# Kernel tuning notes

Hardware: AMD Instinct MI355X
Metric: run time of the kernel (lower is better)

The kernel has to match this reference:

```python
import jax, jax.numpy as jnp
import numpy as np

B, S, H, F, E, K = 2, 2048, 1024, 4096, 8, 2
NH = H // 128  # heads of dim 128, per SimpleMoEBlock.__init__
DH = H // NH


def _layernorm(x, g, b, eps=1e-5):
    m = x.mean(-1, keepdims=True)
    v = ((x - m) ** 2).mean(-1, keepdims=True)
    return (x - m) / jnp.sqrt(v + eps) * g + b


def _forward(x, ln_attn_g, ln_attn_b, ln_mlp_g, ln_mlp_b,
             in_proj_w, in_proj_b, out_proj_w, out_proj_b,
             router_w, fc1_w, fc1_b, fc2_w, fc2_b):
    # --- self attention (nn.MultiheadAttention, batch_first, no mask) ---
    xa = _layernorm(x, ln_attn_g, ln_attn_b)                    # [B,S,H]
    qkv = xa @ in_proj_w.T + in_proj_b                          # [B,S,3H]
    q, k, v = jnp.split(qkv, 3, axis=-1)
    def heads(t):
        return t.reshape(B, S, NH, DH).transpose(0, 2, 1, 3)    # [B,NH,S,DH]
    q, k, v = heads(q), heads(k), heads(v)
    scores = jnp.einsum('bhqd,bhkd->bhqk', q, k) / jnp.sqrt(jnp.asarray(DH, x.dtype))
    attn = jnp.einsum('bhqk,bhkd->bhqd', jax.nn.softmax(scores, axis=-1), v)
    attn = attn.transpose(0, 2, 1, 3).reshape(B, S, H)
    attn = attn @ out_proj_w.T + out_proj_b
    h = x + attn                                                # residual

    # --- MoE feed-forward ---
    y = _layernorm(h, ln_mlp_g, ln_mlp_b).reshape(B * S, H)     # flat tokens [T,H]
    logits = y @ router_w.T                                     # [T,E]
    probs = jax.nn.softmax(logits, axis=-1)
    top_scores, top_idx = jax.lax.top_k(probs, K)               # [T,K]
    # per-token per-expert combine weight; 0 for unrouted tokens -> identical
    # math to torch's index_select/index_add dispatch
    w = (jax.nn.one_hot(top_idx, E, dtype=y.dtype) * top_scores[..., None]).sum(axis=1)  # [T,E]

    combined = jnp.zeros_like(y)
    for e in range(E):  # fixed small expert count
        he = jax.nn.silu(y @ fc1_w[e].T + fc1_b[e])             # [T,F]
        oe = he @ fc2_w[e].T + fc2_b[e]                         # [T,H]
        combined = combined + oe * w[:, e:e + 1]
    return h + combined.reshape(B, S, H)


def setup_inputs() -> dict:
    key = jax.random.key(0)
    ks = jax.random.split(key, 8)
    s = 0.02
    return {
        'x': jax.random.normal(ks[0], (B, S, H), jnp.float32),
        'ln_attn_g': jnp.ones((H,), jnp.float32),
        'ln_attn_b': jnp.zeros((H,), jnp.float32),
        'ln_mlp_g': jnp.ones((H,), jnp.float32),
        'ln_mlp_b': jnp.zeros((H,), jnp.float32),
        'in_proj_w': jax.random.normal(ks[1], (3 * H, H), jnp.float32) * s,
        'in_proj_b': jnp.zeros((3 * H,), jnp.float32),
        'out_proj_w': jax.random.normal(ks[2], (H, H), jnp.float32) * s,
        'out_proj_b': jnp.zeros((H,), jnp.float32),
        'router_w': jax.random.normal(ks[3], (E, H), jnp.float32) * s,
        'fc1_w': jax.random.normal(ks[4], (E, F, H), jnp.float32) * s,
        'fc1_b': jnp.zeros((E, F), jnp.float32),
        'fc2_w': jax.random.normal(ks[5], (E, H, F), jnp.float32) * s,
        'fc2_b': jnp.zeros((E, H), jnp.float32),
    }


def reference(x, ln_attn_g, ln_attn_b, ln_mlp_g, ln_mlp_b,
              in_proj_w, in_proj_b, out_proj_w, out_proj_b,
              router_w, fc1_w, fc1_b, fc2_w, fc2_b):
    return _forward(x, ln_attn_g, ln_attn_b, ln_mlp_g, ln_mlp_b,
                    in_proj_w, in_proj_b, out_proj_w, out_proj_b,
                    router_w, fc1_w, fc1_b, fc2_w, fc2_b)
```

## Files before the change

kernel.cpp:

```cpp
#include <hip/hip_runtime.h>

#define T_TOK 4096
#define S_SEQ 2048
#define H_DIM 1024
#define H3    3072
#define NHEAD 8
#define DHEAD 128
#define F_DIM 4096
#define NEXP  8
#define MAX_RB 72
#define NSLOT 9216

typedef __bf16 bf16x8 __attribute__((ext_vector_type(8)));
typedef float  f32x4  __attribute__((ext_vector_type(4)));
typedef __attribute__((address_space(1))) const unsigned int* gas1_t;
typedef __attribute__((address_space(3))) unsigned int* las3_t;

__device__ __forceinline__ unsigned short f2bf(float f){
  unsigned int u = __builtin_bit_cast(unsigned int, f);
  u += 0x7fffu + ((u>>16)&1u);
  return (unsigned short)(u>>16);
}
__device__ __forceinline__ float bf2f(unsigned short h){
  unsigned int u = ((unsigned int)h)<<16;
  return __builtin_bit_cast(float, u);
}
__device__ __forceinline__ f32x4 MF(bf16x8 a, bf16x8 b, f32x4 c){
  return __builtin_amdgcn_mfma_f32_16x16x32_bf16(a,b,c,0,0,0);
}
__device__ __forceinline__ void gload16(const void* g, void* l){
  __builtin_amdgcn_global_load_lds((gas1_t)g, (las3_t)l, 16, 0, 0);
}
__device__ __forceinline__ float blockReduceSum(float v){
  __shared__ float sh_red[4];
  #pragma unroll
  for(int o=32;o>0;o>>=1) v += __shfl_down(v,o,64);
  int w = threadIdx.x>>6;
  if((threadIdx.x&63)==0) sh_red[w]=v;
  __syncthreads();
  float tot = sh_red[0]+sh_red[1]+sh_red[2]+sh_red[3];
  __syncthreads();
  return tot;
}

__global__ __launch_bounds__(256) void k_ln_split(const float* __restrict__ x,
    const float* __restrict__ g, const float* __restrict__ bta,
    unsigned short* __restrict__ hi, unsigned short* __restrict__ lo){
  int t = blockIdx.x, tid = threadIdx.x;
  float4 v = reinterpret_cast<const float4*>(x + (size_t)t*H_DIM)[tid];
  float mean = blockReduceSum(v.x+v.y+v.z+v.w) * (1.0f/H_DIM);
  float d0=v.x-mean,d1=v.y-mean,d2=v.z-mean,d3=v.w-mean;
  float var = blockReduceSum(d0*d0+d1*d1+d2*d2+d3*d3) * (1.0f/H_DIM);
  float rstd = rsqrtf(var + 1e-5f);
  float4 gv = reinterpret_cast<const float4*>(g)[tid];
  float4 bv = reinterpret_cast<const float4*>(bta)[tid];
  float o0=d0*rstd*gv.x+bv.x, o1=d1*rstd*gv.y+bv.y, o2=d2*rstd*gv.z+bv.z, o3=d3*rstd*gv.w+bv.w;
  size_t base = (size_t)t*H_DIM + tid*4;
  unsigned short h0=f2bf(o0),h1=f2bf(o1),h2=f2bf(o2),h3=f2bf(o3);
  *reinterpret_cast<ushort4*>(hi+base) = make_ushort4(h0,h1,h2,h3);
  *reinterpret_cast<ushort4*>(lo+base) = make_ushort4(
      f2bf(o0-bf2f(h0)), f2bf(o1-bf2f(h1)), f2bf(o2-bf2f(h2)), f2bf(o3-bf2f(h3)));
}

__global__ __launch_bounds__(256) void k_wsplit(const float* __restrict__ w,
    unsigned short* __restrict__ hi, unsigned short* __restrict__ lo, int n4){
  int i = blockIdx.x*256 + threadIdx.x;
  if(i>=n4) return;
  float4 v = reinterpret_cast<const float4*>(w)[i];
  size_t base = (size_t)i*4;
  unsigned short h0=f2bf(v.x),h1=f2bf(v.y),h2=f2bf(v.z),h3=f2bf(v.w);
  *reinterpret_cast<ushort4*>(hi+base) = make_ushort4(h0,h1,h2,h3);
  *reinterpret_cast<ushort4*>(lo+base) = make_ushort4(
      f2bf(v.x-bf2f(h0)), f2bf(v.y-bf2f(h1)), f2bf(v.z-bf2f(h2)), f2bf(v.w-bf2f(h3)));
}

__global__ __launch_bounds__(256) void k_wconv(const float* __restrict__ w,
    unsigned short* __restrict__ hi, int n4){
  int i = blockIdx.x*256 + threadIdx.x;
  if(i>=n4) return;
  float4 v = reinterpret_cast<const float4*>(w)[i];
  *reinterpret_cast<ushort4*>(hi + (size_t)i*4) =
      make_ushort4(f2bf(v.x), f2bf(v.y), f2bf(v.z), f2bf(v.w));
}

template<int EPI>
__global__ __launch_bounds__(256) void k_gemm_split(
    const unsigned short* __restrict__ Ah, const unsigned short* __restrict__ Al,
    const unsigned short* __restrict__ Bh, const unsigned short* __restrict__ Bl,
    const float* __restrict__ bias, const float* __restrict__ resid,
    unsigned short* __restrict__ Chi, unsigned short* __restrict__ Clo,
    float* __restrict__ Cf, int N, int Kd){
  int m0 = blockIdx.y*128, n0 = blockIdx.x*128;
  int tid=threadIdx.x, wid=tid>>6, lane=tid&63, lr=lane&15, lg=lane>>4;
  int wr=wid>>1, wc=wid&1;
  __shared__ unsigned short tAh[4096], tAl[4096], tBh[4096], tBl[4096];
  f32x4 acc[4][4] = {};
  for(int k0=0;k0<Kd;k0+=32){
    #pragma unroll
    for(int i=0;i<2;i++){
      int p = i*256 + tid;
      int row = p>>2, pc = p&3;
      int lc = pc ^ ((row>>1)&3);
      size_t go = (size_t)row*Kd + k0 + lc*8;
      int lb = (i*256 + wid*64)*8;
      gload16(Ah + (size_t)m0*Kd + go, tAh + lb);
      gload16(Al + (size_t)m0*Kd + go, tAl + lb);
      gload16(Bh + (size_t)n0*Kd + go, tBh + lb);
      gload16(Bl + (size_t)n0*Kd + go, tBl + lb);
    }
    asm volatile("s_waitcnt vmcnt(0)" ::: "memory");
    __syncthreads();
    bf16x8 ah[4], al[4], bh[4], bl[4];
    #pragma unroll
    for(int q=0;q<4;q++){
      int ra = wr*64+q*16+lr;
      int ia = ra*32 + ((lg ^ ((ra>>1)&3))<<3);
      ah[q] = *reinterpret_cast<const bf16x8*>(&tAh[ia]);
      al[q] = *reinterpret_cast<const bf16x8*>(&tAl[ia]);
      int rb = wc*64+q*16+lr;
      int ib = rb*32 + ((lg ^ ((rb>>1)&3))<<3);
      bh[q] = *reinterpret_cast<const bf16x8*>(&tBh[ib]);
      bl[q] = *reinterpret_cast<const bf16x8*>(&tBl[ib]);
    }
    #pragma unroll
    for(int mf=0;mf<4;mf++)
      #pragma unroll
      for(int nf=0;nf<4;nf++){
        acc[mf][nf] = MF(ah[mf], bh[nf], acc[mf][nf]);
        acc[mf][nf] = MF(ah[mf], bl[nf], acc[mf][nf]);
        acc[mf][nf] = MF(al[mf], bh[nf], acc[mf][nf]);
      }
    __syncthreads();
  }
  #pragma unroll
  for(int mf=0;mf<4;mf++)
    #pragma unroll
    for(int nf=0;nf<4;nf++)
      #pragma unroll
      for(int r=0;r<4;r++){
        int row = m0 + wr*64 + mf*16 + lg*4 + r;
        int col = n0 + wc*64 + nf*16 + lr;
        float v = acc[mf][nf][r] + bias[col];
        size_t idx = (size_t)row*N + col;
        if(EPI==0){
          unsigned short hb = f2bf(v);
          Chi[idx]=hb; Clo[idx]=f2bf(v-bf2f(hb));
        } else {
          Cf[idx] = v + resid[idx];
        }
      }
}

__global__ __launch_bounds__(256) void k_vtrans(const unsigned short* __restrict__ qh,
    const unsigned short* __restrict__ ql,
    unsigned short* __restrict__ vth, unsigned short* __restrict__ vtl){
  int bh = blockIdx.z, d0 = blockIdx.y*32, s0 = blockIdx.x*32;
  int b = bh>>3, hh = bh&7;
  int tid=threadIdx.x;
  __shared__ unsigned short th[32][40], tl[32][40];
  int sr = tid>>3, dc = (tid&7)*4;
  size_t src = ((size_t)(b*S_SEQ + s0 + sr))*H3 + 2*H_DIM + hh*DHEAD + d0 + dc;
  *reinterpret_cast<ushort4*>(&th[sr][dc]) = *reinterpret_cast<const ushort4*>(qh+src);
  *reinterpret_cast<ushort4*>(&tl[sr][dc]) = *reinterpret_cast<const ushort4*>(ql+src);
  __syncthreads();
  int dr = tid>>3, sc = (tid&7)*4;
  size_t dst = ((size_t)(bh*DHEAD) + d0+dr)*S_SEQ + s0 + sc;
  *reinterpret_cast<ushort4*>(vth+dst) = make_ushort4(th[sc][dr],th[sc+1][dr],th[sc+2][dr],th[sc+3][dr]);
  *reinterpret_cast<ushort4*>(vtl+dst) = make_ushort4(tl[sc][dr],tl[sc+1][dr],tl[sc+2][dr],tl[sc+3][dr]);
}

__global__ __launch_bounds__(256,1) void k_attn(const unsigned short* __restrict__ qkv_hi,
    const unsigned short* __restrict__ qkv_lo,
    const unsigned short* __restrict__ vt_hi, const unsigned short* __restrict__ vt_lo,
    float* __restrict__ opb, float* __restrict__ mlb, int kv_span){
  const float SCALE = 0.08838834764831843f;
  int qb = blockIdx.x, bh = blockIdx.y, zz = blockIdx.z;
  int b = bh>>3, hh = bh&7;
  int kvbase = zz*kv_span, kvend = kvbase + kv_span;
  int tid=threadIdx.x, wid=tid>>6, lane=tid&63, lr=lane&15, lg=lane>>4;
  __shared__ unsigned short kh[2][4096], kl[2][4096], vh[2][4096], vl[2][4096];
  __shared__ unsigned short ph[4][1024], pl[4][1024];
  int row0 = qb*128 + wid*32;
  bf16x8 qh_[2][4], ql_[2][4];
  #pragma unroll
  for(int j=0;j<2;j++){
    size_t qbase = ((size_t)(b*S_SEQ) + row0 + j*16 + lr)*H3 + hh*DHEAD;
    #pragma unroll
    for(int kk=0;kk<4;kk++){
      qh_[j][kk] = *reinterpret_cast<const bf16x8*>(qkv_hi + qbase + kk*32 + lg*8);
      ql_[j][kk] = *reinterpret_cast<const bf16x8*>(qkv_lo + qbase + kk*32 + lg*8);
    }
  }
  f32x4 o_acc[2][8] = {};
  float mrun[2] = {-1e30f,-1e30f};
  float lrun[2] = {0.f,0.f};

  auto STAGE = [&](int buf, int kv0){
    #pragma unroll
    for(int i=0;i<2;i++){
      int p = i*256 + tid;
      int lb = (i*256 + wid*64)*8;
      {
        int krow = p>>4, pc = p&15;
        int lc = (pc&8)|((pc&7)^(krow&7));
        size_t go = ((size_t)(b*S_SEQ + kv0 + krow))*H3 + H_DIM + hh*DHEAD + lc*8;
        gload16(qkv_hi + go, &kh[buf][lb]);
        gload16(qkv_lo + go, &kl[buf][lb]);
      }
      {
        int vrow = p>>2, pc = p&3;
        int lc = pc ^ ((vrow>>1)&3);
        size_t gv = ((size_t)(bh*DHEAD) + vrow)*S_SEQ + kv0 + lc*8;
        gload16(vt_hi + gv, &vh[buf][lb]);
        gload16(vt_lo + gv, &vl[buf][lb]);
      }
    }
  };

  STAGE(0, kvbase);
  asm volatile("s_waitcnt vmcnt(0)" ::: "memory");
  __syncthreads();
  int cur = 0;
  for(int kv0=kvbase; kv0<kvend; kv0+=32){
    if(kv0+32 < kvend) STAGE(cur^1, kv0+32);
    f32x4 s0[2] = {}, s1[2] = {};
    #pragma unroll
    for(int kk=0;kk<4;kk++){
      int c = kk*4+lg;
      int phys = (c&8)|((c&7)^(lr&7));
      bf16x8 kah = *reinterpret_cast<const bf16x8*>(&kh[cur][lr*128 + phys*8]);
      bf16x8 kal = *reinterpret_cast<const bf16x8*>(&kl[cur][lr*128 + phys*8]);
      bf16x8 kbh = *reinterpret_cast<const bf16x8*>(&kh[cur][(16+lr)*128 + phys*8]);
      bf16x8 kbl = *reinterpret_cast<const bf16x8*>(&kl[cur][(16+lr)*128 + phys*8]);
      #pragma unroll
      for(int j=0;j<2;j++){
        s0[j] = MF(kah, qh_[j][kk], s0[j]);
        s0[j] = MF(kah, ql_[j][kk], s0[j]);
        s0[j] = MF(kal, qh_[j][kk], s0[j]);
        s1[j] = MF(kbh, qh_[j][kk], s1[j]);
        s1[j] = MF(kbh, ql_[j][kk], s1[j]);
        s1[j] = MF(kbl, qh_[j][kk], s1[j]);
      }
    }
    float sc[2][8]; float mt[2];
    #pragma unroll
    for(int j=0;j<2;j++){
      #pragma unroll
      for(int r=0;r<4;r++){ sc[j][r] = s0[j][r]*SCALE; sc[j][4+r] = s1[j][r]*SCALE; }
      float m_ = fmaxf(fmaxf(fmaxf(sc[j][0],sc[j][1]),fmaxf(sc[j][2],sc[j][3])),
                       fmaxf(fmaxf(sc[j][4],sc[j][5]),fmaxf(sc[j][6],sc[j][7])));
      m_ = fmaxf(m_, __shfl_xor(m_,16,64));
      m_ = fmaxf(m_, __shfl_xor(m_,32,64));
      mt[j] = m_;
    }
    int skip = __all((mt[0] <= mrun[0]+8.0f) && (mt[1] <= mrun[1]+8.0f));
    if(!skip){
      #pragma unroll
      for(int j=0;j<2;j++){
        float mn = fmaxf(mrun[j], mt[j]);
        float rs = __expf(mrun[j]-mn);
        lrun[j] *= rs; mrun[j] = mn;
        #pragma unroll
        for(int nf2=0;nf2<8;nf2++){
          f32x4 t = o_acc[j][nf2];
          t[0]*=rs; t[1]*=rs; t[2]*=rs; t[3]*=rs;
          o_acc[j][nf2] = t;
        }
      }
    }
    #pragma unroll
    for(int j=0;j<2;j++){
      float ssum = 0.f;
      #pragma unroll
      for(int i=0;i<8;i++){ sc[j][i] = __expf(sc[j][i]-mrun[j]); ssum += sc[j][i]; }
      ssum += __shfl_xor(ssum,16,64);
      ssum += __shfl_xor(ssum,32,64);
      lrun[j] += ssum;
      unsigned short hbk[8], lbk[8];
      #pragma unroll
      for(int i=0;i<8;i++){ hbk[i]=f2bf(sc[j][i]); lbk[i]=f2bf(sc[j][i]-bf2f(hbk[i])); }
      int half = (lg&1)*4;
      int a0 = j*512 + lr*32 + (((lg>>1)^(lr&3))<<3) + half;
      int a1 = j*512 + lr*32 + ((((lg>>1)+2)^(lr&3))<<3) + half;
      *reinterpret_cast<ushort4*>(&ph[wid][a0]) = make_ushort4(hbk[0],hbk[1],hbk[2],hbk[3]);
      *reinterpret_cast<ushort4*>(&pl[wid][a0]) = make_ushort4(lbk[0],lbk[1],lbk[2],lbk[3]);
      *reinterpret_cast<ushort4*>(&ph[wid][a1]) = make_ushort4(hbk[4],hbk[5],hbk[6],hbk[7]);
      *reinterpret_cast<ushort4*>(&pl[wid][a1]) = make_ushort4(lbk[4],lbk[5],lbk[6],lbk[7]);
    }
    bf16x8 pbh[2], pbl[2];
    #pragma unroll
    for(int j=0;j<2;j++){
      int pp = (lg^(lr&3))<<3;
      pbh[j] = *reinterpret_cast<const bf16x8*>(&ph[wid][j*512 + lr*32 + pp]);
      pbl[j] = *reinterpret_cast<const bf16x8*>(&pl[wid][j*512 + lr*32 + pp]);
    }
    #pragma unroll
    for(int nf2=0;nf2<8;nf2++){
      int d = nf2*16 + lr;
      int vp = (lg ^ ((lr>>1)&3))<<3;
      bf16x8 vah = *reinterpret_cast<const bf16x8*>(&vh[cur][d*32 + vp]);
      bf16x8 val = *reinterpret_cast<const bf16x8*>(&vl[cur][d*32 + vp]);
      #pragma unroll
      for(int j=0;j<2;j++){
        o_acc[j][nf2] = MF(vah, pbh[j], o_acc[j][nf2]);
        o_acc[j][nf2] = MF(vah, pbl[j], o_acc[j][nf2]);
        o_acc[j][nf2] = MF(val, pbh[j], o_acc[j][nf2]);
      }
    }
    asm volatile("s_waitcnt vmcnt(0)" ::: "memory");
    __syncthreads();
    cur ^= 1;
  }
  #pragma unroll
  for(int j=0;j<2;j++){
    int srow = row0 + j*16 + lr;
    size_t obase = (((size_t)zz*16 + bh)*S_SEQ + srow)*(size_t)DHEAD;
    #pragma unroll
    for(int nf2=0;nf2<8;nf2++){
      *reinterpret_cast<f32x4*>(&opb[obase + nf2*16 + lg*4]) = o_acc[j][nf2];
    }
    if(lg==0){
      *reinterpret_cast<float2*>(&mlb[(((size_t)zz*16 + bh)*S_SEQ + srow)*2]) =
          make_float2(mrun[j], lrun[j]);
    }
  }
}

__global__ __launch_bounds__(256) void k_amerge(const float* __restrict__ opb,
    const float* __restrict__ mlb, int nz,
    unsigned short* __restrict__ o_hi, unsigned short* __restrict__ o_lo){
  int bh = blockIdx.y, b = bh>>3, hh = bh&7;
  int r = threadIdx.x>>4;
  int c = (threadIdx.x&15)*8;
  int srow = blockIdx.x*16 + r;
  float mz[2], lz[2];
  float m = -1e30f;
  for(int z=0;z<nz;z++){
    const float* mlp = mlb + (((size_t)z*16 + bh)*S_SEQ + srow)*2;
    mz[z]=mlp[0]; lz[z]=mlp[1];
    m = fmaxf(m, mz[z]);
  }
  float L = 0.f, w[2];
  for(int z=0;z<nz;z++){ w[z] = __expf(mz[z]-m); L += lz[z]*w[z]; }
  float linv = 1.0f/L;
  float acc[8] = {0,0,0,0,0,0,0,0};
  for(int z=0;z<nz;z++){
    const float* o = opb + (((size_t)z*16 + bh)*S_SEQ + srow)*(size_t)DHEAD + c;
    float4 a = *reinterpret_cast<const float4*>(o);
    float4 bq = *reinterpret_cast<const float4*>(o+4);
    acc[0]+=a.x*w[z]; acc[1]+=a.y*w[z]; acc[2]+=a.z*w[z]; acc[3]+=a.w*w[z];
    acc[4]+=bq.x*w[z]; acc[5]+=bq.y*w[z]; acc[6]+=bq.z*w[z]; acc[7]+=bq.w*w[z];
  }
  size_t idx = ((size_t)(b*S_SEQ)+srow)*H_DIM + hh*DHEAD + c;
  unsigned short hp[8], lp[8];
  #pragma unroll
  for(int i=0;i<8;i++){
    float v = acc[i]*linv;
    hp[i]=f2bf(v); lp[i]=f2bf(v-bf2f(hp[i]));
  }
  *reinterpret_cast<ushort4*>(o_hi+idx)   = make_ushort4(hp[0],hp[1],hp[2],hp[3]);
  *reinterpret_cast<ushort4*>(o_hi+idx+4) = make_ushort4(hp[4],hp[5],hp[6],hp[7]);
  *reinterpret_cast<ushort4*>(o_lo+idx)   = make_ushort4(lp[0],lp[1],lp[2],lp[3]);
  *reinterpret_cast<ushort4*>(o_lo+idx+4) = make_ushort4(lp[4],lp[5],lp[6],lp[7]);
}

__global__ __launch_bounds__(256) void k_ln2_router(const float* __restrict__ h,
    const float* __restrict__ g, const float* __restrict__ bt, const float* __restrict__ rw,
    unsigned short* __restrict__ ybf, int* __restrict__ route_e, float* __restrict__ route_w){
  int t = blockIdx.x, tid = threadIdx.x;
  float4 v = reinterpret_cast<const float4*>(h + (size_t)t*H_DIM)[tid];
  float mean = blockReduceSum(v.x+v.y+v.z+v.w) * (1.0f/H_DIM);
  float d0=v.x-mean,d1=v.y-mean,d2=v.z-mean,d3=v.w-mean;
  float var = blockReduceSum(d0*d0+d1*d1+d2*d2+d3*d3) * (1.0f/H_DIM);
  float rstd = rsqrtf(var + 1e-5f);
  float4 gv = reinterpret_cast<const float4*>(g)[tid];
  float4 bv = reinterpret_cast<const float4*>(bt)[tid];
  float o0=d0*rstd*gv.x+bv.x, o1=d1*rstd*gv.y+bv.y, o2=d2*rstd*gv.z+bv.z, o3=d3*rstd*gv.w+bv.w;
  size_t base = (size_t)t*H_DIM + tid*4;
  *reinterpret_cast<ushort4*>(ybf+base) = make_ushort4(f2bf(o0),f2bf(o1),f2bf(o2),f2bf(o3));
  float part[8];
  #pragma unroll
  for(int e=0;e<8;e++){
    float4 r = reinterpret_cast<const float4*>(rw + e*H_DIM)[tid];
    part[e] = o0*r.x + o1*r.y + o2*r.z + o3*r.w;
  }
  __shared__ float sm[32];
  #pragma unroll
  for(int e=0;e<8;e++){
    float p = part[e];
    #pragma unroll
    for(int o=32;o>0;o>>=1) p += __shfl_down(p,o,64);
    if((tid&63)==0) sm[(tid>>6)*8+e] = p;
  }
  __syncthreads();
  if(tid==0){
    float lgt[8];
    #pragma unroll
    for(int e=0;e<8;e++) lgt[e] = sm[e]+sm[8+e]+sm[16+e]+sm[24+e];
    float mx = lgt[0];
    #pragma unroll
    for(int e=1;e<8;e++) mx = fmaxf(mx, lgt[e]);
    float ex[8], ssum=0.f;
    #pragma unroll
    for(int e=0;e<8;e++){ ex[e]=__expf(lgt[e]-mx); ssum+=ex[e]; }
    float inv = 1.0f/ssum;
    int e0=0; float p0=ex[0];
    for(int e=1;e<8;e++) if(ex[e]>p0){p0=ex[e];e0=e;}
    int e1=-1; float p1=-1.0f;
    for(int e=0;e<8;e++) if(e!=e0 && ex[e]>p1){p1=ex[e];e1=e;}
    route_e[2*t]=e0; route_e[2*t+1]=e1;
    route_w[2*t]=p0*inv; route_w[2*t+1]=p1*inv;
  }
}

__global__ __launch_bounds__(256) void k_compact(const int* __restrict__ route_e,
    const float* __restrict__ route_w, int* __restrict__ tok_of_slot,
    float* __restrict__ w_of_slot, int* __restrict__ slot_of_tok,
    int* __restrict__ rb_expert, int* __restrict__ rb_base){
  __shared__ int cnt[8], off[8], pos[8];
  int tid = threadIdx.x;
  if(tid<8){ cnt[tid]=0; pos[tid]=0; }
  __syncthreads();
  for(int t=tid;t<T_TOK;t+=256){
    atomicAdd(&cnt[route_e[2*t]],1);
    atomicAdd(&cnt[route_e[2*t+1]],1);
  }
  __syncthreads();
  if(tid==0){
    int o=0;
    for(int e=0;e<8;e++){ off[e]=o; o += ((cnt[e]+127)>>7)<<7; }
    int rb=0;
    for(int e=0;e<8;e++){
      int nrb = (cnt[e]+127)>>7;
      for(int r=0;r<nrb;r++){ rb_expert[rb]=e; rb_base[rb]=off[e]+r*128; rb++; }
    }
    for(;rb<MAX_RB;rb++){ rb_expert[rb]=-1; rb_base[rb]=0; }
  }
  __syncthreads();
  for(int s=tid;s<NSLOT;s+=256){ tok_of_slot[s]=0; w_of_slot[s]=0.0f; }
  __syncthreads();
  for(int t=tid;t<T_TOK;t+=256){
    int e0=route_e[2*t], e1=route_e[2*t+1];
    int s0 = off[e0] + atomicAdd(&pos[e0],1);
    tok_of_slot[s0]=t; w_of_slot[s0]=route_w[2*t]; slot_of_tok[2*t]=s0;
    int s1 = off[e1] + atomicAdd(&pos[e1],1);
    tok_of_slot[s1]=t; w_of_slot[s1]=route_w[2*t+1]; slot_of_tok[2*t+1]=s1;
  }
}

template<bool FC1, bool PRE>
__global__ __launch_bounds__(256) void k_fc(const unsigned short* __restrict__ Abuf,
    const float* __restrict__ W, const unsigned short* __restrict__ Wbf,
    const float* __restrict__ bias,
    const int* __restrict__ rb_expert, const int* __restrict__ rb_base,
    const int* __restrict__ tok_of_slot, const float* __restrict__ w_of_slot,
    unsigned short* __restrict__ he_out, float* __restrict__ oew_out){
  int rb = blockIdx.y;
  int e = rb_expert[rb];
  if(e<0) return;
  int base = rb_base[rb];
  int n0 = blockIdx.x*128;
  const int Kd = FC1 ? H_DIM : F_DIM;
  const int Nd = FC1 ? F_DIM : H_DIM;
  int tid=threadIdx.x, wid=tid>>6, lane=tid&63, lr=lane&15, lg=lane>>4;
  int wr=wid>>1, wc=wid&1;
  __shared__ unsigned short tA[4096], tB[4096];
  size_t arow_src[2];
  #pragma unroll
  for(int i=0;i<2;i++){
    int row = i*64 + (tid>>2);
    if(FC1){ int tok = tok_of_slot[base+row]; arow_src[i] = (size_t)tok*H_DIM; }
    else   { arow_src[i] = (size_t)(base+row)*F_DIM; }
  }
  const float* Wp = W + (size_t)e*F_DIM*H_DIM;
  const unsigned short* Wbp = Wbf + (size_t)e*F_DIM*H_DIM;
  f32x4 acc[4][4] = {};
  for(int k0=0;k0<Kd;k0+=32){
    #pragma unroll
    for(int i=0;i<2;i++){
      int p = i*256+tid; int row=p>>2, pc=p&3;
      int lc = pc ^ ((row>>1)&3);
      gload16(Abuf + arow_src[i] + k0 + lc*8, tA + (i*256+wid*64)*8);
      if(PRE){
        gload16(Wbp + (size_t)(n0+row)*Kd + k0 + lc*8, tB + (i*256+wid*64)*8);
      }
    }
    if(!PRE){
      #pragma unroll
      for(int j=0;j<4;j++){
        int f = tid*16 + j*4; int row=f>>5; int kin=f&31;
        float4 wv = *reinterpret_cast<const float4*>(Wp + (size_t)(n0+row)*Kd + k0 + kin);
        int c16 = kin>>3, half=(kin>>2)&1;
        int phys = c16 ^ ((row>>1)&3);
        *reinterpret_cast<ushort4*>(&tB[row*32 + phys*8 + half*4]) =
            make_ushort4(f2bf(wv.x), f2bf(wv.y), f2bf(wv.z), f2bf(wv.w));
      }
    }
    asm volatile("s_waitcnt vmcnt(0)" ::: "memory");
    __syncthreads();
    bf16x8 af[4], bfr[4];
    #pragma unroll
    for(int q=0;q<4;q++){
      int ra = wr*64+q*16+lr;
      af[q] = *reinterpret_cast<const bf16x8*>(&tA[ra*32 + ((lg ^ ((ra>>1)&3))<<3)]);
      int rbw = wc*64+q*16+lr;
      bfr[q] = *reinterpret_cast<const bf16x8*>(&tB[rbw*32 + ((lg ^ ((rbw>>1)&3))<<3)]);
    }
    #pragma unroll
    for(int mf=0;mf<4;mf++)
      #pragma unroll
      for(int nf=0;nf<4;nf++)
        acc[mf][nf] = MF(af[mf], bfr[nf], acc[mf][nf]);
    __syncthreads();
  }
  #pragma unroll
  for(int mf=0;mf<4;mf++)
    #pragma unroll
    for(int nf=0;nf<4;nf++)
      #pragma unroll
      for(int r=0;r<4;r++){
        int lrow = wr*64+mf*16+lg*4+r;
        int col = n0 + wc*64+nf*16+lr;
        float v = acc[mf][nf][r] + bias[(size_t)e*Nd + col];
        if(FC1){
          float sv = v/(1.0f+__expf(-v));
          he_out[(size_t)(base+lrow)*F_DIM + col] = f2bf(sv);
        } else {
          oew_out[(size_t)(base+lrow)*H_DIM + col] = w_of_slot[base+lrow]*v;
        }
      }
}

__global__ __launch_bounds__(256) void k_combine(const float* __restrict__ h,
    const float* __restrict__ oew, const int* __restrict__ slot_of_tok,
    float* __restrict__ out){
  int t = blockIdx.x, tid=threadIdx.x;
  int s0 = slot_of_tok[2*t], s1 = slot_of_tok[2*t+1];
  float4 hv = reinterpret_cast<const float4*>(h + (size_t)t*H_DIM)[tid];
  float4 a = reinterpret_cast<const float4*>(oew + (size_t)s0*H_DIM)[tid];
  float4 b = reinterpret_cast<const float4*>(oew + (size_t)s1*H_DIM)[tid];
  float4 o = make_float4(hv.x+a.x+b.x, hv.y+a.y+b.y, hv.z+a.z+b.z, hv.w+a.w+b.w);
  reinterpret_cast<float4*>(out + (size_t)t*H_DIM)[tid] = o;
}

extern "C" void kernel_launch(void* const* d_in, const int* in_sizes, int n_in,
                              void* d_out, int out_size, void* d_ws, size_t ws_size,
                              hipStream_t stream){
  const float* x    = (const float*)d_in[0];
  const float* ln1g = (const float*)d_in[1];
  const float* ln1b = (const float*)d_in[2];
  const float* ln2g = (const float*)d_in[3];
  const float* ln2b = (const float*)d_in[4];
  const float* wqkv = (const float*)d_in[5];
  const float* bqkv = (const float*)d_in[6];
  const float* wout = (const float*)d_in[7];
  const float* bout = (const float*)d_in[8];
  const float* rw   = (const float*)d_in[9];
  const float* fc1w = (const float*)d_in[10];
  const float* fc1b = (const float*)d_in[11];
  const float* fc2w = (const float*)d_in[12];
  const float* fc2b = (const float*)d_in[13];
  char* ws = (char*)d_ws;

  size_t off_ = 0;
  auto AL = [&](size_t bytes){ size_t r = off_; off_ = (off_ + bytes + 255) & ~(size_t)255; return r; };
  size_t o_xa_hi = AL((size_t)T_TOK*H_DIM*2), o_xa_lo = AL((size_t)T_TOK*H_DIM*2);
  size_t o_wq_hi = AL((size_t)H3*H_DIM*2),    o_wq_lo = AL((size_t)H3*H_DIM*2);
  size_t o_wo_hi = AL((size_t)H_DIM*H_DIM*2), o_wo_lo = AL((size_t)H_DIM*H_DIM*2);
  size_t o_qk_hi = AL((size_t)T_TOK*H3*2),    o_qk_lo = AL((size_t)T_TOK*H3*2);
  size_t o_vt_hi = AL((size_t)16*DHEAD*S_SEQ*2), o_vt_lo = AL((size_t)16*DHEAD*S_SEQ*2);
  size_t o_at_hi = AL((size_t)T_TOK*H_DIM*2), o_at_lo = AL((size_t)T_TOK*H_DIM*2);
  size_t o_he  = 0;
  size_t o_oew = (size_t)NSLOT*F_DIM*2;
  size_t o_h   = AL((size_t)T_TOK*H_DIM*4);
  size_t o_ybf = AL((size_t)T_TOK*H_DIM*2);
  size_t o_re  = AL((size_t)T_TOK*2*4);
  size_t o_rwt = AL((size_t)T_TOK*2*4);
  size_t o_st  = AL((size_t)T_TOK*2*4);
  size_t o_ts  = AL((size_t)NSLOT*4);
  size_t o_wsl = AL((size_t)NSLOT*4);
  size_t o_rbe = AL(4096);
  size_t o_rbb = AL(4096);
  size_t o_wb  = AL((size_t)NEXP*F_DIM*H_DIM*2);
  bool pre = (off_ <= ws_size);
  size_t o_op  = AL((size_t)2*16*S_SEQ*DHEAD*4 + (size_t)2*16*S_SEQ*2*4 + 256);
  bool pre2 = (off_ <= ws_size);
  (void)in_sizes; (void)n_in; (void)out_size;

  unsigned short* xa_hi = (unsigned short*)(ws+o_xa_hi);
  unsigned short* xa_lo = (unsigned short*)(ws+o_xa_lo);
  unsigned short* wq_hi = (unsigned short*)(ws+o_wq_hi);
  unsigned short* wq_lo = (unsigned short*)(ws+o_wq_lo);
  unsigned short* wo_hi = (unsigned short*)(ws+o_wo_hi);
  unsigned short* wo_lo = (unsigned short*)(ws+o_wo_lo);
  unsigned short* qk_hi = (unsigned short*)(ws+o_qk_hi);
  unsigned short* qk_lo = (unsigned short*)(ws+o_qk_lo);
  unsigned short* vt_hi = (unsigned short*)(ws+o_vt_hi);
  unsigned short* vt_lo = (unsigned short*)(ws+o_vt_lo);
  unsigned short* at_hi = (unsigned short*)(ws+o_at_hi);
  unsigned short* at_lo = (unsigned short*)(ws+o_at_lo);
  unsigned short* he    = (unsigned short*)(ws+o_he);
  float* oew   = (float*)(ws+o_oew);
  float* hbuf  = (float*)(ws+o_h);
  unsigned short* ybf = (unsigned short*)(ws+o_ybf);
  int*   route_e = (int*)(ws+o_re);
  float* route_w = (float*)(ws+o_rwt);
  int*   slot_of_tok = (int*)(ws+o_st);
  int*   tok_of_slot = (int*)(ws+o_ts);
  float* w_of_slot   = (float*)(ws+o_wsl);
  int*   rb_expert   = (int*)(ws+o_rbe);
  int*   rb_base     = (int*)(ws+o_rbb);
  unsigned short* wb = (unsigned short*)(ws+o_wb);

  int nz = pre2 ? 2 : 1;
  float* opb = pre2 ? (float*)(ws+o_op) : (float*)(ws+o_xa_hi);
  float* mlb = opb + (size_t)nz*16*S_SEQ*DHEAD;

  k_ln_split<<<T_TOK, 256, 0, stream>>>(x, ln1g, ln1b, xa_hi, xa_lo);
  k_wsplit<<<(H3*H_DIM/4+255)/256, 256, 0, stream>>>(wqkv, wq_hi, wq_lo, H3*H_DIM/4);
  k_wsplit<<<(H_DIM*H_DIM/4+255)/256, 256, 0, stream>>>(wout, wo_hi, wo_lo, H_DIM*H_DIM/4);
  k_gemm_split<0><<<dim3(H3/128, T_TOK/128), 256, 0, stream>>>(
      xa_hi, xa_lo, wq_hi, wq_lo, bqkv, nullptr, qk_hi, qk_lo, nullptr, H3, H_DIM);
  k_vtrans<<<dim3(S_SEQ/32, DHEAD/32, 16), 256, 0, stream>>>(qk_hi, qk_lo, vt_hi, vt_lo);
  k_attn<<<dim3(S_SEQ/128, 16, nz), 256, 0, stream>>>(qk_hi, qk_lo, vt_hi, vt_lo,
                                                      opb, mlb, S_SEQ/nz);
  k_amerge<<<dim3(S_SEQ/16, 16), 256, 0, stream>>>(opb, mlb, nz, at_hi, at_lo);
  k_gemm_split<1><<<dim3(H_DIM/128, T_TOK/128), 256, 0, stream>>>(
      at_hi, at_lo, wo_hi, wo_lo, bout, x, nullptr, nullptr, hbuf, H_DIM, H_DIM);
  k_ln2_router<<<T_TOK, 256, 0, stream>>>(hbuf, ln2g, ln2b, rw, ybf, route_e, route_w);
  k_compact<<<1, 256, 0, stream>>>(route_e, route_w, tok_of_slot, w_of_slot,
                                   slot_of_tok, rb_expert, rb_base);
  const int WN4 = NEXP*F_DIM*H_DIM/4;
  if(pre){
    k_wconv<<<(WN4+255)/256, 256, 0, stream>>>(fc1w, wb, WN4);
    k_fc<true,true><<<dim3(F_DIM/128, MAX_RB), 256, 0, stream>>>(
        ybf, fc1w, wb, fc1b, rb_expert, rb_base, tok_of_slot, nullptr, he, nullptr);
    k_wconv<<<(WN4+255)/256, 256, 0, stream>>>(fc2w, wb, WN4);
    k_fc<false,true><<<dim3(H_DIM/128, MAX_RB), 256, 0, stream>>>(
        he, fc2w, wb, fc2b, rb_expert, rb_base, tok_of_slot, w_of_slot, nullptr, oew);
  } else {
    k_fc<true,false><<<dim3(F_DIM/128, MAX_RB), 256, 0, stream>>>(
        ybf, fc1w, wb, fc1b, rb_expert, rb_base, tok_of_slot, nullptr, he, nullptr);
    k_fc<false,false><<<dim3(H_DIM/128, MAX_RB), 256, 0, stream>>>(
        he, fc2w, wb, fc2b, rb_expert, rb_base, tok_of_slot, w_of_slot, nullptr, oew);
  }
  k_combine<<<T_TOK, 256, 0, stream>>>(hbuf, oew, slot_of_tok, (float*)d_out);
}
```

Baseline: 736.2 us.

## Single-buffer attention K/V staging to fit two blocks per CU

Drops the double-buffered K/V shared memory tiles in the attention kernel in favour of a single buffer loaded and waited on at the start of each iteration. The launch-bounds hint changes to request two blocks per CU. The aim is to hide memory latency through extra occupancy instead of software prefetch, at the cost of exposing load latency within each block and tighter register limits. The V swizzle index now uses d rather than lr, which is equivalent because nf2*16 leaves (d>>1)&3 unchanged.

```diff
diff --git a/kernel.cpp b/kernel.cpp
--- a/kernel.cpp
+++ b/kernel.cpp
@@ -169,7 +169,7 @@
   *reinterpret_cast<ushort4*>(vtl+dst) = make_ushort4(tl[sc][dr],tl[sc+1][dr],tl[sc+2][dr],tl[sc+3][dr]);
 }
 
-__global__ __launch_bounds__(256,1) void k_attn(const unsigned short* __restrict__ qkv_hi,
+__global__ __launch_bounds__(256,2) void k_attn(const unsigned short* __restrict__ qkv_hi,
     const unsigned short* __restrict__ qkv_lo,
     const unsigned short* __restrict__ vt_hi, const unsigned short* __restrict__ vt_lo,
     float* __restrict__ opb, float* __restrict__ mlb, int kv_span){
@@ -178,7 +178,7 @@
   int b = bh>>3, hh = bh&7;
   int kvbase = zz*kv_span, kvend = kvbase + kv_span;
   int tid=threadIdx.x, wid=tid>>6, lane=tid&63, lr=lane&15, lg=lane>>4;
-  __shared__ unsigned short kh[2][4096], kl[2][4096], vh[2][4096], vl[2][4096];
+  __shared__ unsigned short kh[4096], kl[4096], vh[4096], vl[4096];
   __shared__ unsigned short ph[4][1024], pl[4][1024];
   int row0 = qb*128 + wid*32;
   bf16x8 qh_[2][4], ql_[2][4];
@@ -195,7 +195,7 @@
   float mrun[2] = {-1e30f,-1e30f};
   float lrun[2] = {0.f,0.f};
 
-  auto STAGE = [&](int buf, int kv0){
+  auto STAGE = [&](int kv0){
     #pragma unroll
     for(int i=0;i<2;i++){
       int p = i*256 + tid;
@@ -204,34 +204,32 @@
         int krow = p>>4, pc = p&15;
         int lc = (pc&8)|((pc&7)^(krow&7));
         size_t go = ((size_t)(b*S_SEQ + kv0 + krow))*H3 + H_DIM + hh*DHEAD + lc*8;
-        gload16(qkv_hi + go, &kh[buf][lb]);
-        gload16(qkv_lo + go, &kl[buf][lb]);
+        gload16(qkv_hi + go, &kh[lb]);
+        gload16(qkv_lo + go, &kl[lb]);
       }
       {
         int vrow = p>>2, pc = p&3;
         int lc = pc ^ ((vrow>>1)&3);
         size_t gv = ((size_t)(bh*DHEAD) + vrow)*S_SEQ + kv0 + lc*8;
-        gload16(vt_hi + gv, &vh[buf][lb]);
-        gload16(vt_lo + gv, &vl[buf][lb]);
+        gload16(vt_hi + gv, &vh[lb]);
+        gload16(vt_lo + gv, &vl[lb]);
       }
     }
   };
 
-  STAGE(0, kvbase);
-  asm volatile("s_waitcnt vmcnt(0)" ::: "memory");
-  __syncthreads();
-  int cur = 0;
   for(int kv0=kvbase; kv0<kvend; kv0+=32){
-    if(kv0+32 < kvend) STAGE(cur^1, kv0+32);
+    STAGE(kv0);
+    asm volatile("s_waitcnt vmcnt(0)" ::: "memory");
+    __syncthreads();
     f32x4 s0[2] = {}, s1[2] = {};
     #pragma unroll
     for(int kk=0;kk<4;kk++){
       int c = kk*4+lg;
       int phys = (c&8)|((c&7)^(lr&7));
-      bf16x8 kah = *reinterpret_cast<const bf16x8*>(&kh[cur][lr*128 + phys*8]);
-      bf16x8 kal = *reinterpret_cast<const bf16x8*>(&kl[cur][lr*128 + phys*8]);
-      bf16x8 kbh = *reinterpret_cast<const bf16x8*>(&kh[cur][(16+lr)*128 + phys*8]);
-      bf16x8 kbl = *reinterpret_cast<const bf16x8*>(&kl[cur][(16+lr)*128 + phys*8]);
+      bf16x8 kah = *reinterpret_cast<const bf16x8*>(&kh[lr*128 + phys*8]);
+      bf16x8 kal = *reinterpret_cast<const bf16x8*>(&kl[lr*128 + phys*8]);
+      bf16x8 kbh = *reinterpret_cast<const bf16x8*>(&kh[(16+lr)*128 + phys*8]);
+      bf16x8 kbl = *reinterpret_cast<const bf16x8*>(&kl[(16+lr)*128 + phys*8]);
       #pragma unroll
       for(int j=0;j<2;j++){
         s0[j] = MF(kah, qh_[j][kk], s0[j]);
@@ -297,9 +295,9 @@
     #pragma unroll
     for(int nf2=0;nf2<8;nf2++){
       int d = nf2*16 + lr;
-      int vp = (lg ^ ((lr>>1)&3))<<3;
-      bf16x8 vah = *reinterpret_cast<const bf16x8*>(&vh[cur][d*32 + vp]);
-      bf16x8 val = *reinterpret_cast<const bf16x8*>(&vl[cur][d*32 + vp]);
+      int vp = (lg ^ ((d>>1)&3))<<3;
+      bf16x8 vah = *reinterpret_cast<const bf16x8*>(&vh[d*32 + vp]);
+      bf16x8 val = *reinterpret_cast<const bf16x8*>(&vl[d*32 + vp]);
       #pragma unroll
       for(int j=0;j<2;j++){
         o_acc[j][nf2] = MF(vah, pbh[j], o_acc[j][nf2]);
@@ -307,9 +305,7 @@
         o_acc[j][nf2] = MF(val, pbh[j], o_acc[j][nf2]);
       }
     }
-    asm volatile("s_waitcnt vmcnt(0)" ::: "memory");
     __syncthreads();
-    cur ^= 1;
   }
   #pragma unroll
   for(int j=0;j<2;j++){
```

Result: faster. 679.1 us (-7.7%).
